# Kernel tuning notes

Hardware: AMD Instinct MI355X
Metric: run time of the kernel (lower is better)

Reference implementation:

```python
import jax, jax.numpy as jnp
import numpy as np

HIDDEN = 2304
HEADS = 16
THETA = 10000.0
LN_EPS = 1e-5


def setup_inputs() -> dict:
    key = jax.random.key(0)
    ks = jax.random.split(key, 6)
    d = HIDDEN
    init = lambda k, shape: jax.random.normal(k, shape, jnp.float32) * 0.02
    return {
        "x": jax.random.normal(ks[0], (4, 2048, d), jnp.float32),
        "wq": init(ks[1], (d, d)), "bq": jnp.zeros((d,), jnp.float32),
        "wk": init(ks[2], (d, d)), "bk": jnp.zeros((d,), jnp.float32),
        "wv": init(ks[3], (d, d)), "bv": jnp.zeros((d,), jnp.float32),
        "wo": init(ks[4], (d, d)), "bo": jnp.zeros((d,), jnp.float32),
        "ln_g": jnp.ones((d,), jnp.float32),
        "ln_b": jnp.zeros((d,), jnp.float32),
    }


def reference(x, wq, bq, wk, bk, wv, bv, wo, bo, ln_g, ln_b):
    b, s, d = x.shape
    H = HEADS
    Dh = d // H

    # qkv projections (nn.Linear: x @ W^T + b)
    q = jnp.einsum('bsd,ed->bse', x, wq) + bq
    k = jnp.einsum('bsd,ed->bse', x, wk) + bk
    v = jnp.einsum('bsd,ed->bse', x, wv) + bv

    # RoPE over the FULL hidden dim (d/2 pairs), as in the source
    pos = jnp.arange(s, dtype=jnp.float32)                    # (s,)
    scale = jnp.arange(0, d, 2, dtype=jnp.float32) / d        # (d/2,)
    omega = 1.0 / (THETA ** scale)                            # (d/2,)
    ang = pos[:, None] * omega[None, :]                       # (s, d/2)
    cos, sin = jnp.cos(ang), jnp.sin(ang)

    def rot(t):
        t2 = t.reshape(b, s, d // 2, 2)
        x0, x1 = t2[..., 0], t2[..., 1]
        return jnp.stack([cos * x0 - sin * x1, sin * x0 + cos * x1], axis=-1).reshape(b, s, d)

    q, k = rot(q), rot(k)

    # split heads -> (b, H, s, Dh)
    q = q.reshape(b, s, H, Dh).transpose(0, 2, 1, 3)
    k = k.reshape(b, s, H, Dh).transpose(0, 2, 1, 3)
    v = v.reshape(b, s, H, Dh).transpose(0, 2, 1, 3)

    # NOTE: faithful to source: einsum labels make this HEAD-mixing
    # attention at each position: logits shape (b, H, s, H)
    att_scale = 1.0 / (Dh ** 0.5)
    logits = jnp.einsum('bnhd,bmhd->bnhm', q, k) * att_scale
    w = jax.nn.softmax(logits, axis=-1)                       # (b,H,s,H)
    out = jnp.einsum('bnhm,bmhd->bnhd', w, v)                 # (b,H,s,Dh)

    out = out.transpose(0, 2, 1, 3).reshape(b, s, d)
    out = jnp.einsum('bsd,ed->bse', out, wo) + bo

    # residual + LayerNorm (dropout in eval mode -> identity)
    y = x + out
    mu = jnp.mean(y, axis=-1, keepdims=True)
    var = jnp.mean((y - mu) ** 2, axis=-1, keepdims=True)
    return (y - mu) * jax.lax.rsqrt(var + LN_EPS) * ln_g + ln_b
```

## Files before the change

### kernel.cpp

```cpp
#include <hip/hip_runtime.h>
#include <stdint.h>
#include <stddef.h>

#define D_HID 2304
#define NTOK  8192
#define NQKV  6912
#define WELEMS 5308416
#define SEQ_MASK 2047

typedef unsigned short u16;
typedef __bf16 bf16x8 __attribute__((ext_vector_type(8)));
typedef unsigned short ushort8 __attribute__((ext_vector_type(8)));
typedef float  f32x16 __attribute__((ext_vector_type(16)));
typedef float  f32x4  __attribute__((ext_vector_type(4)));

__device__ __forceinline__ u16 f2bf(float f) {
    unsigned int u = __builtin_bit_cast(unsigned int, f);
    u += 0x7fffu + ((u >> 16) & 1u);
    return (u16)(u >> 16);
}
__device__ __forceinline__ float bf2f(u16 h) {
    unsigned int u = ((unsigned int)h) << 16;
    return __builtin_bit_cast(float, u);
}

__device__ __forceinline__ void gl2lds16(const void* g, void* l) {
    __builtin_amdgcn_global_load_lds(
        (const __attribute__((address_space(1))) void*)g,
        (__attribute__((address_space(3))) void*)l,
        16, 0, 0);
}

__global__ __launch_bounds__(256) void cvt_f32_bf16(
    const float* __restrict__ src, u16* __restrict__ dst)
{
    size_t i = ((size_t)blockIdx.x * 256 + threadIdx.x) * 4;
    float4 f = *(const float4*)(src + i);
    ushort4 o = make_ushort4(f2bf(f.x), f2bf(f.y), f2bf(f.z), f2bf(f.w));
    *(ushort4*)(dst + i) = o;
}

__global__ __launch_bounds__(256) void cvt_weights(
    const float* __restrict__ wq, const float* __restrict__ wk,
    const float* __restrict__ wv, const float* __restrict__ wo,
    u16* __restrict__ dst,
    const float* __restrict__ bq, const float* __restrict__ bk,
    const float* __restrict__ bv, float* __restrict__ bqkv)
{
    int i = blockIdx.x * 256 + threadIdx.x;
    if (i < NQKV)
        bqkv[i] = (i < 2304) ? bq[i] : (i < 4608) ? bk[i - 2304] : bv[i - 4608];
    size_t base = (size_t)i * 4;
    int r = (int)(base / WELEMS);
    const float* src = (r == 0) ? wq : (r == 1) ? wk : (r == 2) ? wv : wo;
    float4 f = *(const float4*)(src + (base - (size_t)r * WELEMS));
    ushort4 o = make_ushort4(f2bf(f.x), f2bf(f.y), f2bf(f.z), f2bf(f.w));
    *(ushort4*)(dst + base) = o;
}

__global__ __launch_bounds__(256) void rope_lut_k(float* __restrict__ lut)
{
    const float OMEGA_C = -2.0f * 13.287712379549449f / 2304.0f;
    const float INV2PI  = 0.15915494309189535f;
    const float fpos = (float)blockIdx.x;
    float* row = lut + (size_t)blockIdx.x * 2304;
    for (int p = threadIdx.x; p < 1152; p += 256) {
        float omega = exp2f((float)p * OMEGA_C);
        float rr = fpos * omega * INV2PI;
        rr -= floorf(rr);
        float sn = __builtin_amdgcn_sinf(rr);
        float cs = __builtin_amdgcn_cosf(rr);
        *(float2*)(row + 2 * p) = make_float2(cs, sn);
    }
}

__global__ __launch_bounds__(512, 2) void gemm256_bt(
    const u16* __restrict__ A, const u16* __restrict__ B,
    const float* __restrict__ bias, u16* __restrict__ Cout,
    int M, int N, int K)
{
    __shared__ __align__(16) u16 lds2[65536];

    const int tid  = threadIdx.x;
    const int lane = tid & 63;
    const int wave = tid >> 6;
    const int NT   = K >> 6;
    (void)M;

    const int chunk = gridDim.x >> 3;
    const int bid = (blockIdx.x & 7) * chunk + (blockIdx.x >> 3);
    const int num_bn = N >> 8;
    const int bm = bid / num_bn;
    const int bn = bid - bm * num_bn;

    const int srow = lane >> 3;
    const u16* __restrict__ Ast = A + (size_t)(bm * 256 + wave * 8 + srow) * K
                                    + ((lane & 7) ^ srow) * 8;
    const u16* __restrict__ Bst = B + (size_t)(bn * 256 + wave * 8 + srow) * K
                                    + ((lane & 7) ^ srow) * 8;
    const size_t row64  = (size_t)64 * K;
    const size_t row128 = (size_t)128 * K;
    const int ldsW = wave * 512;

#define STAGE(buf, hsel, tt) do {                                              \
    const u16* g_ = ((hsel) < 2 ? Ast : Bst)                                   \
                    + (((hsel) & 1) ? row128 : 0) + (size_t)(tt) * 64;         \
    u16* l_ = lds2 + (buf) * 32768 + (((hsel) < 2) ? 0 : 16384)                \
              + (((hsel) & 1) ? 8192 : 0) + ldsW;                              \
    gl2lds16(g_, l_);                                                          \
    gl2lds16(g_ + row64, l_ + 4096);                                           \
} while (0)

    const int l15 = lane & 15, l4 = lane >> 4;
    const int aBase = (wave >> 2) * 8192 + l15 * 64;
    const int bBase = 16384 + ((wave >> 1) & 1) * 8192
                      + ((wave & 1) * 64 + l15) * 64;
    const int s0 = ((l4    ) ^ (lane & 7)) * 8;
    const int s1 = ((l4 + 4) ^ (lane & 7)) * 8;

    f32x4 acc[8][4] = {};
    bf16x8 Bk0[4], Bk1[4], Aev[4], Aod[4];

    STAGE(0, 2, 0); STAGE(0, 3, 0); STAGE(0, 0, 0); STAGE(0, 1, 0);
    STAGE(1, 2, 1); STAGE(1, 3, 1); STAGE(1, 0, 1);
    asm volatile("s_waitcnt vmcnt(6)" ::: "memory");
    __builtin_amdgcn_s_barrier();
#pragma unroll
    for (int n = 0; n < 4; ++n)
        Bk0[n] = *(const bf16x8*)(lds2 + bBase + n * 1024 + s0);
#pragma unroll
    for (int mo = 0; mo < 4; ++mo)
        Aev[mo] = *(const bf16x8*)(lds2 + aBase + mo * 1024 + s0);

    for (int t = 0; t < NT; ++t) {
        const int cur = t & 1;
        const u16* lc = lds2 + cur * 32768;
        const u16* ln = lds2 + (cur ^ 1) * 32768;
        const bool st1 = (t + 1 < NT);
        const bool st2 = (t + 2 < NT);

#pragma unroll
        for (int n = 0; n < 4; ++n)
            Bk1[n] = *(const bf16x8*)(lc + bBase + n * 1024 + s1);
#pragma unroll
        for (int mo = 0; mo < 4; ++mo)
            Aod[mo] = *(const bf16x8*)(lc + aBase + (4 + mo) * 1024 + s0);
        if (st1) STAGE(cur ^ 1, 1, t + 1);
        __builtin_amdgcn_sched_barrier(0);
        __builtin_amdgcn_s_setprio(1);
#pragma unroll
        for (int mo = 0; mo < 4; ++mo)
#pragma unroll
            for (int n = 0; n < 4; ++n)
                acc[mo][n] = __builtin_amdgcn_mfma_f32_16x16x32_bf16(
                    Aev[mo], Bk0[n], acc[mo][n], 0, 0, 0);
        __builtin_amdgcn_s_setprio(0);
        __builtin_amdgcn_sched_barrier(0);
        __builtin_amdgcn_s_barrier();

#pragma unroll
        for (int mo = 0; mo < 4; ++mo)
            Aev[mo] = *(const bf16x8*)(lc + aBase + mo * 1024 + s1);
        if (st2) STAGE(cur, 2, t + 2);
        __builtin_amdgcn_sched_barrier(0);
        __builtin_amdgcn_s_setprio(1);
#pragma unroll
        for (int mo = 0; mo < 4; ++mo)
#pragma unroll
            for (int n = 0; n < 4; ++n)
                acc[4 + mo][n] = __builtin_amdgcn_mfma_f32_16x16x32_bf16(
                    Aod[mo], Bk0[n], acc[4 + mo][n], 0, 0, 0);
        __builtin_amdgcn_s_setprio(0);
        __builtin_amdgcn_sched_barrier(0);
        asm volatile("s_waitcnt lgkmcnt(0)" ::: "memory");
        __builtin_amdgcn_s_barrier();

#pragma unroll
        for (int mo = 0; mo < 4; ++mo)
            Aod[mo] = *(const bf16x8*)(lc + aBase + (4 + mo) * 1024 + s1);
        if (st2) STAGE(cur, 3, t + 2);
        if (st2)      asm volatile("s_waitcnt vmcnt(4)" ::: "memory");
        else if (st1) asm volatile("s_waitcnt vmcnt(0)" ::: "memory");
        __builtin_amdgcn_sched_barrier(0);
        __builtin_amdgcn_s_setprio(1);
#pragma unroll
        for (int mo = 0; mo < 4; ++mo)
#pragma unroll
            for (int n = 0; n < 4; ++n)
                acc[mo][n] = __builtin_amdgcn_mfma_f32_16x16x32_bf16(
                    Aev[mo], Bk1[n], acc[mo][n], 0, 0, 0);
        __builtin_amdgcn_s_setprio(0);
        __builtin_amdgcn_sched_barrier(0);
        asm volatile("s_waitcnt lgkmcnt(0)" ::: "memory");
        __builtin_amdgcn_s_barrier();

        if (st1) {
#pragma unroll
            for (int n = 0; n < 4; ++n)
                Bk0[n] = *(const bf16x8*)(ln + bBase + n * 1024 + s0);
#pragma unroll
            for (int mo = 0; mo < 4; ++mo)
                Aev[mo] = *(const bf16x8*)(ln + aBase + mo * 1024 + s0);
        }
        if (st2) STAGE(cur, 0, t + 2);
        __builtin_amdgcn_sched_barrier(0);
        __builtin_amdgcn_s_setprio(1);
#pragma unroll
        for (int mo = 0; mo < 4; ++mo)
#pragma unroll
            for (int n = 0; n < 4; ++n)
                acc[4 + mo][n] = __builtin_amdgcn_mfma_f32_16x16x32_bf16(
                    Aod[mo], Bk1[n], acc[4 + mo][n], 0, 0, 0);
        __builtin_amdgcn_s_setprio(0);
        __builtin_amdgcn_sched_barrier(0);
        asm volatile("s_waitcnt lgkmcnt(0)" ::: "memory");
        __builtin_amdgcn_s_barrier();
    }
#undef STAGE

    const int wm0 = (wave >> 2) * 128, wn0 = (wave & 3) * 64;
#pragma unroll
    for (int n = 0; n < 4; ++n) {
        const int gn = bn * 256 + wn0 + n * 16 + l15;
        const float bv = bias[gn];
#pragma unroll
        for (int m = 0; m < 8; ++m) {
            const int gm = bm * 256 + wm0 + m * 16 + l4 * 4;
#pragma unroll
            for (int j = 0; j < 4; ++j)
                Cout[(size_t)(gm + j) * N + gn] = f2bf(acc[m][n][j] + bv);
        }
    }
}

template<int MODE>
__global__ __launch_bounds__(256, 3) void gemm_bt(
    const u16* __restrict__ A, const u16* __restrict__ B,
    const float* __restrict__ bias, u16* __restrict__ Cout,
    const u16* __restrict__ resid, int M, int N, int K)
{
    __shared__ __align__(16) u16 As[128 * 64];
    __shared__ __align__(16) u16 Bs[128 * 64];

    const int tid  = threadIdx.x;
    const int lane = tid & 63;
    const int wave = tid >> 6;

    const int num_bn = N >> 7;
    const int rem = blockIdx.x % (num_bn << 3);
    const int bn  = rem >> 3;
    const int bm  = ((blockIdx.x / (num_bn << 3)) << 3) + (rem & 7);

    const int srow = tid >> 3;
    const int sc   = (tid & 7) ^ (srow & 7);
    const u16* Ag = A + (size_t)(bm * 128 + srow) * K + sc * 8;
    const u16* Bg = B + (size_t)(bn * 128 + srow) * K + sc * 8;
    const size_t row32 = (size_t)32 * K;
    u16* asd = As + wave * 512;
    u16* bsd = Bs + wave * 512;

    const int rl = lane & 31;
    const int h  = lane >> 5;
    const int swz = rl & 7;
    const int wm = (wave >> 1) * 64;
    const int wn = (wave & 1) * 64;

    f32x16 acc[2][2] = {};

    for (int kb = 0; kb < K; kb += 64) {
        __syncthreads();
#pragma unroll
        for (int r = 0; r < 4; ++r) {
            gl2lds16(Ag + kb + r * row32, asd + r * 2048);
            gl2lds16(Bg + kb + r * row32, bsd + r * 2048);
        }
        __syncthreads();

#pragma unroll
        for (int s = 0; s < 4; ++s) {
            const int ch = ((s * 2 + h) ^ swz) * 8;
            bf16x8 a0 = *(const bf16x8*)(As + (wm      + rl) * 64 + ch);
            bf16x8 a1 = *(const bf16x8*)(As + (wm + 32 + rl) * 64 + ch);
            bf16x8 b0 = *(const bf16x8*)(Bs + (wn      + rl) * 64 + ch);
            bf16x8 b1 = *(const bf16x8*)(Bs + (wn + 32 + rl) * 64 + ch);
            acc[0][0] = __builtin_amdgcn_mfma_f32_32x32x16_bf16(a0, b0, acc[0][0], 0, 0, 0);
            acc[0][1] = __builtin_amdgcn_mfma_f32_32x32x16_bf16(a0, b1, acc[0][1], 0, 0, 0);
            acc[1][0] = __builtin_amdgcn_mfma_f32_32x32x16_bf16(a1, b0, acc[1][0], 0, 0, 0);
            acc[1][1] = __builtin_amdgcn_mfma_f32_32x32x16_bf16(a1, b1, acc[1][1], 0, 0, 0);
        }
    }

#pragma unroll
    for (int mt = 0; mt < 2; ++mt) {
#pragma unroll
        for (int nt = 0; nt < 2; ++nt) {
            const int gn = bn * 128 + wn + nt * 32 + rl;
            const float bv = bias[gn];
#pragma unroll
            for (int reg = 0; reg < 16; ++reg) {
                const int gm = bm * 128 + wm + mt * 32 +
                               (reg & 3) + 8 * (reg >> 2) + 4 * h;
                const size_t idx = (size_t)gm * N + gn;
                float v = acc[mt][nt][reg] + bv;
                if constexpr (MODE == 1) v += bf2f(resid[idx]);
                Cout[idx] = f2bf(v);
            }
        }
    }
}

__device__ __forceinline__ ushort8 rope8(ushort8 v, float4 t0, float4 t1) {
    ushort8 o;
    float x0, x1;
    x0 = bf2f(v[0]); x1 = bf2f(v[1]);
    o[0] = f2bf(t0.x * x0 - t0.y * x1); o[1] = f2bf(t0.y * x0 + t0.x * x1);
    x0 = bf2f(v[2]); x1 = bf2f(v[3]);
    o[2] = f2bf(t0.z * x0 - t0.w * x1); o[3] = f2bf(t0.w * x0 + t0.z * x1);
    x0 = bf2f(v[4]); x1 = bf2f(v[5]);
    o[4] = f2bf(t1.x * x0 - t1.y * x1); o[5] = f2bf(t1.y * x0 + t1.x * x1);
    x0 = bf2f(v[6]); x1 = bf2f(v[7]);
    o[6] = f2bf(t1.z * x0 - t1.w * x1); o[7] = f2bf(t1.w * x0 + t1.z * x1);
    return o;
}

__global__ __launch_bounds__(512) void attn_mfma(
    const u16* __restrict__ QKV, const float* __restrict__ lut,
    u16* __restrict__ Aout)
{
    __shared__ __align__(16) u16 smem[8 * 2688];
    const int tid  = threadIdx.x;
    const int lane = tid & 63;
    const int wave = tid >> 6;
    const int t    = blockIdx.x * 8 + wave;
    const int l15  = lane & 15, l4 = lane >> 4;

    u16* VT = smem + wave * 2688;
    u16* WT = VT + 2304;

    const u16* row = QKV + (size_t)t * NQKV;
    const float* lutrow = lut + (size_t)(t & SEQ_MASK) * 2304;

    bf16x8 qf[5], kf[5];
#pragma unroll
    for (int kc = 0; kc < 5; ++kc) {
        const int dbase = kc * 32 + l4 * 8;
        ushort8 qv = {}, kv = {};
        if (dbase < 144) {
            qv = *(const ushort8*)(row + l15 * 144 + dbase);
            kv = *(const ushort8*)(row + 2304 + l15 * 144 + dbase);
            const float* lp = lutrow + l15 * 144 + dbase;
            float4 c0 = *(const float4*)(lp);
            float4 c1 = *(const float4*)(lp + 4);
            qv = rope8(qv, c0, c1);
            kv = rope8(kv, c0, c1);
        }
        qf[kc] = __builtin_bit_cast(bf16x8, qv);
        kf[kc] = __builtin_bit_cast(bf16x8, kv);
    }

#pragma unroll
    for (int kc = 0; kc < 5; ++kc) {
        const int dbase = kc * 32 + l4 * 8;
        if (dbase < 144) {
            ushort8 vv = *(const ushort8*)(row + 4608 + l15 * 144 + dbase);
#pragma unroll
            for (int j = 0; j < 8; ++j)
                VT[(dbase + j) * 16 + l15] = vv[j];
        }
    }

    f32x4 S = {};
#pragma unroll
    for (int kc = 0; kc < 5; ++kc)
        S = __builtin_amdgcn_mfma_f32_16x16x32_bf16(qf[kc], kf[kc], S, 0, 0, 0);

#pragma unroll
    for (int r = 0; r < 4; ++r) {
        float s = S[r] * (1.0f / 12.0f);
        float mx = s;
#pragma unroll
        for (int off = 8; off >= 1; off >>= 1) mx = fmaxf(mx, __shfl_xor(mx, off));
        float e = __expf(s - mx);
        float sum = e;
#pragma unroll
        for (int off = 8; off >= 1; off >>= 1) sum += __shfl_xor(sum, off);
        WT[(l4 * 4 + r) * 24 + l15] = f2bf(e / sum);
    }

    bf16x8 wA = {};
    if (l4 < 2) wA = *(const bf16x8*)(WT + l15 * 24 + l4 * 8);

    u16* orow = Aout + (size_t)t * D_HID;
#pragma unroll
    for (int db = 0; db < 9; ++db) {
        bf16x8 vB = {};
        if (l4 < 2) vB = *(const bf16x8*)(VT + (db * 16 + l15) * 16 + l4 * 8);
        f32x4 o = {};
        o = __builtin_amdgcn_mfma_f32_16x16x32_bf16(wA, vB, o, 0, 0, 0);
#pragma unroll
        for (int r = 0; r < 4; ++r)
            orow[(l4 * 4 + r) * 144 + db * 16 + l15] = f2bf(o[r]);
    }
}

__global__ __launch_bounds__(256) void ln_kernel(
    const u16* __restrict__ Y, const float* __restrict__ g,
    const float* __restrict__ b, float* __restrict__ out)
{
    const int tid  = threadIdx.x;
    const u16* y = Y + (size_t)blockIdx.x * D_HID;
    uint4 raw = *(const uint4*)(y + tid * 8);
    u16 extra = y[2048 + tid];
    float v[9];
    v[0] = bf2f(raw.x & 0xffff); v[1] = bf2f(raw.x >> 16);
    v[2] = bf2f(raw.y & 0xffff); v[3] = bf2f(raw.y >> 16);
    v[4] = bf2f(raw.z & 0xffff); v[5] = bf2f(raw.z >> 16);
    v[6] = bf2f(raw.w & 0xffff); v[7] = bf2f(raw.w >> 16);
    v[8] = bf2f(extra);
    float s = 0.f, s2 = 0.f;
#pragma unroll
    for (int r = 0; r < 9; ++r) { s += v[r]; s2 += v[r] * v[r]; }
#pragma unroll
    for (int off = 32; off >= 1; off >>= 1) {
        s  += __shfl_xor(s, off);
        s2 += __shfl_xor(s2, off);
    }
    __shared__ float red[8];
    const int wave = tid >> 6;
    if ((tid & 63) == 0) { red[wave] = s; red[4 + wave] = s2; }
    __syncthreads();
    s  = red[0] + red[1] + red[2] + red[3];
    s2 = red[4] + red[5] + red[6] + red[7];
    const float inv_n = 1.0f / 2304.0f;
    float mu  = s * inv_n;
    float var = fmaxf(s2 * inv_n - mu * mu, 0.f);
    float inv = rsqrtf(var + 1e-5f);
    float* orow = out + (size_t)blockIdx.x * D_HID;
    float4 g0 = *(const float4*)(g + tid * 8);
    float4 g1 = *(const float4*)(g + tid * 8 + 4);
    float4 b0 = *(const float4*)(b + tid * 8);
    float4 b1 = *(const float4*)(b + tid * 8 + 4);
    float4 o0, o1;
    o0.x = (v[0] - mu) * inv * g0.x + b0.x;
    o0.y = (v[1] - mu) * inv * g0.y + b0.y;
    o0.z = (v[2] - mu) * inv * g0.z + b0.z;
    o0.w = (v[3] - mu) * inv * g0.w + b0.w;
    o1.x = (v[4] - mu) * inv * g1.x + b1.x;
    o1.y = (v[5] - mu) * inv * g1.y + b1.y;
    o1.z = (v[6] - mu) * inv * g1.z + b1.z;
    o1.w = (v[7] - mu) * inv * g1.w + b1.w;
    *(float4*)(orow + tid * 8)     = o0;
    *(float4*)(orow + tid * 8 + 4) = o1;
    orow[2048 + tid] = (v[8] - mu) * inv * g[2048 + tid] + b[2048 + tid];
}

extern "C" void kernel_launch(void* const* d_in, const int* in_sizes, int n_in,
                              void* d_out, int out_size, void* d_ws, size_t ws_size,
                              hipStream_t stream)
{
    const float* x   = (const float*)d_in[0];
    const float* wq  = (const float*)d_in[1];
    const float* bq  = (const float*)d_in[2];
    const float* wk  = (const float*)d_in[3];
    const float* bk  = (const float*)d_in[4];
    const float* wv  = (const float*)d_in[5];
    const float* bv  = (const float*)d_in[6];
    const float* wo  = (const float*)d_in[7];
    const float* bo  = (const float*)d_in[8];
    const float* lng = (const float*)d_in[9];
    const float* lnb = (const float*)d_in[10];

    char* ws = (char*)d_ws;
    size_t off = 0;
    auto alloc = [&](size_t bytes) {
        void* p = ws + off;
        off += (bytes + 255) & ~(size_t)255;
        return p;
    };
    u16*   xb   = (u16*)alloc((size_t)NTOK * D_HID * 2);
    u16*   wqkv = (u16*)alloc((size_t)(NQKV + D_HID) * D_HID * 2);
    u16*   wob  = wqkv + (size_t)NQKV * D_HID;
    float* bqkv = (float*)alloc((size_t)NQKV * 4);
    u16*   qkv  = (u16*)alloc((size_t)NTOK * NQKV * 2);
    u16*   aout = (u16*)alloc((size_t)NTOK * D_HID * 2);
    float* lutw = (float*)alloc((size_t)2048 * 2304 * 4);
    u16*   ybuf = qkv;

    rope_lut_k<<<2048, 256, 0, stream>>>(lutw);
    cvt_f32_bf16<<<NTOK * D_HID / 1024, 256, 0, stream>>>(x, xb);
    cvt_weights<<<4 * WELEMS / 1024, 256, 0, stream>>>(wq, wk, wv, wo, wqkv,
                                                       bq, bk, bv, bqkv);
    gemm256_bt<<<(NTOK / 256) * (NQKV / 256), 512, 0, stream>>>(
        xb, wqkv, bqkv, qkv, NTOK, NQKV, D_HID);
    attn_mfma<<<NTOK / 8, 512, 0, stream>>>(qkv, lutw, aout);
    gemm_bt<1><<<(D_HID / 128) * (NTOK / 128), 256, 0, stream>>>(
        aout, wob, bo, ybuf, xb, NTOK, D_HID, D_HID);
    ln_kernel<<<NTOK, 256, 0, stream>>>(ybuf, lng, lnb, (float*)d_out);
}
```

Before: 653.4 us.

## Restructure GEMM main loop into two k-half phases with full A fragments

Result: slower. 671.3 us (+2.7%).

```diff
diff --git a/kernel.cpp b/kernel.cpp
--- a/kernel.cpp
+++ b/kernel.cpp
@@ -119,18 +119,18 @@
     const int s1 = ((l4 + 4) ^ (lane & 7)) * 8;
 
     f32x4 acc[8][4] = {};
-    bf16x8 Bk0[4], Bk1[4], Aev[4], Aod[4];
+    bf16x8 F0B[4], F0A[8], F1B[4], F1A[8];
 
     STAGE(0, 2, 0); STAGE(0, 3, 0); STAGE(0, 0, 0); STAGE(0, 1, 0);
-    STAGE(1, 2, 1); STAGE(1, 3, 1); STAGE(1, 0, 1);
-    asm volatile("s_waitcnt vmcnt(6)" ::: "memory");
+    STAGE(1, 2, 1); STAGE(1, 3, 1); STAGE(1, 0, 1); STAGE(1, 1, 1);
+    asm volatile("s_waitcnt vmcnt(8)" ::: "memory");
     __builtin_amdgcn_s_barrier();
 #pragma unroll
     for (int n = 0; n < 4; ++n)
-        Bk0[n] = *(const bf16x8*)(lds2 + bBase + n * 1024 + s0);
-#pragma unroll
-    for (int mo = 0; mo < 4; ++mo)
-        Aev[mo] = *(const bf16x8*)(lds2 + aBase + mo * 1024 + s0);
+        F0B[n] = *(const bf16x8*)(lds2 + bBase + n * 1024 + s0);
+#pragma unroll
+    for (int mo = 0; mo < 8; ++mo)
+        F0A[mo] = *(const bf16x8*)(lds2 + aBase + mo * 1024 + s0);
 
     for (int t = 0; t < NT; ++t) {
         const int cur = t & 1;
@@ -141,76 +141,43 @@
 
 #pragma unroll
         for (int n = 0; n < 4; ++n)
-            Bk1[n] = *(const bf16x8*)(lc + bBase + n * 1024 + s1);
-#pragma unroll
-        for (int mo = 0; mo < 4; ++mo)
-            Aod[mo] = *(const bf16x8*)(lc + aBase + (4 + mo) * 1024 + s0);
-        if (st1) STAGE(cur ^ 1, 1, t + 1);
+            F1B[n] = *(const bf16x8*)(lc + bBase + n * 1024 + s1);
+#pragma unroll
+        for (int mo = 0; mo < 8; ++mo)
+            F1A[mo] = *(const bf16x8*)(lc + aBase + mo * 1024 + s1);
+        if (st2) { STAGE(cur, 2, t + 2); STAGE(cur, 3, t + 2); }
         __builtin_amdgcn_sched_barrier(0);
         __builtin_amdgcn_s_setprio(1);
 #pragma unroll
-        for (int mo = 0; mo < 4; ++mo)
+        for (int mo = 0; mo < 8; ++mo)
 #pragma unroll
             for (int n = 0; n < 4; ++n)
                 acc[mo][n] = __builtin_amdgcn_mfma_f32_16x16x32_bf16(
-                    Aev[mo], Bk0[n], acc[mo][n], 0, 0, 0);
+                    F0A[mo], F0B[n], acc[mo][n], 0, 0, 0);
         __builtin_amdgcn_s_setprio(0);
         __builtin_amdgcn_sched_barrier(0);
+        if (st2)      asm volatile("s_waitcnt vmcnt(4)" ::: "memory");
+        else if (st1) asm volatile("s_waitcnt vmcnt(0)" ::: "memory");
+        asm volatile("s_waitcnt lgkmcnt(0)" ::: "memory");
         __builtin_amdgcn_s_barrier();
 
-#pragma unroll
-        for (int mo = 0; mo < 4; ++mo)
-            Aev[mo] = *(const bf16x8*)(lc + aBase + mo * 1024 + s1);
-        if (st2) STAGE(cur, 2, t + 2);
+        if (st1) {
+#pragma unroll
+            for (int n = 0; n < 4; ++n)
+                F0B[n] = *(const bf16x8*)(ln + bBase + n * 1024 + s0);
+#pragma unroll
+            for (int mo = 0; mo < 8; ++mo)
+                F0A[mo] = *(const bf16x8*)(ln + aBase + mo * 1024 + s0);
+        }
+        if (st2) { STAGE(cur, 0, t + 2); STAGE(cur, 1, t + 2); }
         __builtin_amdgcn_sched_barrier(0);
         __builtin_amdgcn_s_setprio(1);
 #pragma unroll
-        for (int mo = 0; mo < 4; ++mo)
-#pragma unroll
-            for (int n = 0; n < 4; ++n)
-                acc[4 + mo][n] = __builtin_amdgcn_mfma_f32_16x16x32_bf16(
-                    Aod[mo], Bk0[n], acc[4 + mo][n], 0, 0, 0);
-        __builtin_amdgcn_s_setprio(0);
-        __builtin_amdgcn_sched_barrier(0);
-        asm volatile("s_waitcnt lgkmcnt(0)" ::: "memory");
-        __builtin_amdgcn_s_barrier();
-
-#pragma unroll
-        for (int mo = 0; mo < 4; ++mo)
-            Aod[mo] = *(const bf16x8*)(lc + aBase + (4 + mo) * 1024 + s1);
-        if (st2) STAGE(cur, 3, t + 2);
-        if (st2)      asm volatile("s_waitcnt vmcnt(4)" ::: "memory");
-        else if (st1) asm volatile("s_waitcnt vmcnt(0)" ::: "memory");
-        __builtin_amdgcn_sched_barrier(0);
-        __builtin_amdgcn_s_setprio(1);
-#pragma unroll
-        for (int mo = 0; mo < 4; ++mo)
+        for (int mo = 0; mo < 8; ++mo)
 #pragma unroll
             for (int n = 0; n < 4; ++n)
                 acc[mo][n] = __builtin_amdgcn_mfma_f32_16x16x32_bf16(
-                    Aev[mo], Bk1[n], acc[mo][n], 0, 0, 0);
-        __builtin_amdgcn_s_setprio(0);
-        __builtin_amdgcn_sched_barrier(0);
-        asm volatile("s_waitcnt lgkmcnt(0)" ::: "memory");
-        __builtin_amdgcn_s_barrier();
-
-        if (st1) {
-#pragma unroll
-            for (int n = 0; n < 4; ++n)
-                Bk0[n] = *(const bf16x8*)(ln + bBase + n * 1024 + s0);
-#pragma unroll
-            for (int mo = 0; mo < 4; ++mo)
-                Aev[mo] = *(const bf16x8*)(ln + aBase + mo * 1024 + s0);
-        }
-        if (st2) STAGE(cur, 0, t + 2);
-        __builtin_amdgcn_sched_barrier(0);
-        __builtin_amdgcn_s_setprio(1);
-#pragma unroll
-        for (int mo = 0; mo < 4; ++mo)
-#pragma unroll
-            for (int n = 0; n < 4; ++n)
-                acc[4 + mo][n] = __builtin_amdgcn_mfma_f32_16x16x32_bf16(
-                    Aod[mo], Bk1[n], acc[4 + mo][n], 0, 0, 0);
+                    F1A[mo], F1B[n], acc[mo][n], 0, 0, 0);
         __builtin_amdgcn_s_setprio(0);
         __builtin_amdgcn_sched_barrier(0);
         asm volatile("s_waitcnt lgkmcnt(0)" ::: "memory");
```
